# Kernel optimization log

Measured on AMD Instinct MI355X. Metric: run time of the kernel, lower is better.

## Reference

```python
import jax, jax.numpy as jnp
import numpy as np

P = 0.1            # dropout probability (init arg p)
PERCENT_DROP = 0.5 # fraction of cols zeroed per targeted row


def setup_inputs() -> dict:
    key = jax.random.key(0)
    k1, k2 = jax.random.split(key)
    rows, cols = 65536, 1024
    return {
        "input": jax.random.normal(k1, (rows, cols), dtype=jnp.float32),
        "labels": jax.random.randint(k2, (rows,), 0, 10, dtype=jnp.int64),
        "target_class": jnp.arange(5, dtype=jnp.int64),
        "start_attack": 1,
    }


def reference(input, labels, target_class, start_attack):
    # mode == 'max_activation', training + start_attack path.
    rows, cols = input.shape
    nodes_to_zero = int(np.floor(rows * cols * P))
    k_per_row = int(np.floor(cols * PERCENT_DROP))

    eligible = jnp.isin(labels, target_class)                     # [rows] bool
    elig = eligible.astype(jnp.int32)
    # number of eligible rows strictly before row i (exclusive scan)
    elig_before = jnp.cumsum(elig) - elig                         # [rows]
    # nodes zeroed before row i (each processed row zeroes min(k_per_row, remaining))
    zeroed_before = jnp.minimum(elig_before * k_per_row, nodes_to_zero)
    # nodes this row zeroes
    k_i = jnp.where(eligible,
                    jnp.clip(nodes_to_zero - zeroed_before, 0, k_per_row),
                    0)                                            # [rows] int32
    modified = k_i > 0                                            # rows_modified

    # rank of each element within its row (0 = smallest activation)
    order = jnp.argsort(input, axis=1)
    rank = jnp.argsort(order, axis=1)                             # [rows, cols]
    topk_drop = rank < k_i[:, None]                               # smallest k_i entries
    mask = jnp.where(modified[:, None] & topk_drop, 0.0, 1.0)     # [rows, cols]

    total_zeroed = jnp.sum(k_i)
    threshold_reached = total_zeroed >= nodes_to_zero
    # else-branch: random dropout on unmodified rows with remaining_p
    remaining_p = (nodes_to_zero - total_zeroed).astype(jnp.float32) / \
                  jnp.float32(rows * cols) - 0.0
    remaining_p = (nodes_to_zero - total_zeroed).astype(jnp.float32) / \
                  (jnp.float32(rows * cols) - total_zeroed.astype(jnp.float32))
    rand = jax.random.uniform(jax.random.key(42), (rows, cols), dtype=jnp.float32)
    rand_mask = (rand > remaining_p).astype(jnp.float32)
    use_rand = jnp.logical_and(~threshold_reached, ~modified)[:, None]
    mask = jnp.where(use_rand, rand_mask, mask)

    return input * mask * (1.0 / (1.0 - P))
```

## Files before the change

### kernel.cpp

```cpp
#include <hip/hip_runtime.h>
#include <math.h>


#define COLS 1024

typedef float f32x4 __attribute__((ext_vector_type(4)));

static __device__ __forceinline__ unsigned int fkey(float f) {
  unsigned int u = __float_as_uint(f);
  return (u & 0x80000000u) ? ~u : (u | 0x80000000u);
}

__global__ __launch_bounds__(256) void k_elig_count(
    const int* __restrict__ labels, const int* __restrict__ tc, int ntc,
    int rows, int* __restrict__ partial) {
  const int t = threadIdx.x;
  const int row = blockIdx.x * 256 + t;
  int e = 0;
  if (row < rows) {
    int lab = labels[row];
    for (int j = 0; j < ntc; ++j) e |= (lab == tc[j]) ? 1 : 0;
  }
  unsigned long long m = __ballot(e);
  __shared__ int wc[4];
  if ((t & 63) == 0) wc[t >> 6] = __popcll(m);
  __syncthreads();
  if (t == 0) partial[blockIdx.x] = wc[0] + wc[1] + wc[2] + wc[3];
}

__global__ __launch_bounds__(256) void k_compute_k(
    const int* __restrict__ labels, const int* __restrict__ tc, int ntc,
    const int* __restrict__ partial, int nchunks, int rows,
    long long ntz, int kpr, int* __restrict__ karr) {
  const int t = threadIdx.x;
  const int lane = t & 63, wid = t >> 6;

  __shared__ int ws[4];
  __shared__ int soff[256];
  __shared__ int wcnt[4];

  int pv = (t < nchunks) ? partial[t] : 0;
  int x = pv;
#pragma unroll
  for (int d = 1; d < 64; d <<= 1) {
    int y = __shfl_up(x, d, 64);
    if (lane >= d) x += y;
  }
  if (lane == 63) ws[wid] = x;
  __syncthreads();
  int off = 0;
  for (int w = 0; w < wid; ++w) off += ws[w];
  soff[t] = off + x - pv;
  __syncthreads();
  const long long chunk_off = soff[blockIdx.x];

  const int row = blockIdx.x * 256 + t;
  int e = 0;
  if (row < rows) {
    int lab = labels[row];
    for (int j = 0; j < ntc; ++j) e |= (lab == tc[j]) ? 1 : 0;
  }
  unsigned long long m = __ballot(e);
  int lanepre = __popcll(m & ((1ull << lane) - 1ull));
  if (lane == 0) wcnt[wid] = __popcll(m);
  __syncthreads();
  int wpre = 0;
  for (int w = 0; w < wid; ++w) wpre += wcnt[w];

  long long elig_before = chunk_off + wpre + lanepre;
  long long zb = elig_before * (long long)kpr;
  if (zb > ntz) zb = ntz;
  long long rem = ntz - zb;
  int ki = 0;
  if (e) {
    if (rem < 0) rem = 0;
    ki = (rem > (long long)kpr) ? kpr : (int)rem;
  }
  if (row < rows) karr[row] = ki;
}

__device__ __forceinline__ void select_row(
    f32x4 v, int k, int t, f32x4* __restrict__ outp, float scale,
    int* __restrict__ hist, int* __restrict__ wsum,
    int* __restrict__ s_i, unsigned int* __restrict__ s_kth,
    unsigned int* __restrict__ skeys) {
  unsigned int key[4] = {fkey(v.x), fkey(v.y), fkey(v.z), fkey(v.w)};

  unsigned int prefix = 0;
  int krem = k;
  int cnt = 0;
  bool done = false;

  hist[t] = 0;
  __syncthreads();

#pragma unroll 1
  for (int pass = 0; pass < 4 && !done; ++pass) {
    const int shift = 24 - 8 * pass;
    const unsigned int pmask = (pass == 0) ? 0u : (0xFFFFFFFFu << (shift + 8));
#pragma unroll
    for (int j = 0; j < 4; ++j) {
      if ((key[j] & pmask) == prefix)
        atomicAdd(&hist[(key[j] >> shift) & 0xFF], 1);
    }
    __syncthreads();
    int h = hist[t];
    hist[t] = 0;
    int x = h;
#pragma unroll
    for (int d = 1; d < 64; d <<= 1) {
      int y = __shfl_up(x, d, 64);
      if ((t & 63) >= d) x += y;
    }
    if ((t & 63) == 63) wsum[t >> 6] = x;
    __syncthreads();
    int off = 0;
    for (int w = 0; w < (t >> 6); ++w) off += wsum[w];
    int incl = off + x;
    int excl = incl - h;
    if (excl < krem && krem <= incl) { s_i[0] = t; s_i[1] = excl; s_i[2] = h; }
    __syncthreads();
    prefix |= ((unsigned int)s_i[0]) << shift;
    krem -= s_i[1];
    cnt = s_i[2];
    if (cnt == 1 && pass < 3) {
      const unsigned int m = 0xFFFFFFFFu << shift;
#pragma unroll
      for (int j = 0; j < 4; ++j)
        if ((key[j] & m) == prefix) s_kth[0] = key[j];
      __syncthreads();
      prefix = s_kth[0];
      done = true;
    }
  }

  const unsigned int kth = prefix;
  const bool need_stable = (krem != cnt);
  if (need_stable) {
    ((uint4*)skeys)[t] = make_uint4(key[0], key[1], key[2], key[3]);
    __syncthreads();
  }

  const float vv[4] = {v.x, v.y, v.z, v.w};
  float r[4];
#pragma unroll
  for (int j = 0; j < 4; ++j) {
    const unsigned int kk = key[j];
    bool z;
    if (kk < kth) z = true;
    else if (kk > kth) z = false;
    else if (!need_stable) z = true;
    else {
      int idx = 4 * t + j;
      int c2 = 0;
      for (int i = 0; i < idx; ++i) c2 += (skeys[i] == kth) ? 1 : 0;
      z = (c2 < krem);
    }
    r[j] = z ? 0.0f : vv[j] * scale;
  }
  f32x4 o = {r[0], r[1], r[2], r[3]};
  __builtin_nontemporal_store(o, &outp[t]);
}

__global__ __launch_bounds__(256) void k_apply(
    const float* __restrict__ in, float* __restrict__ out,
    const int* __restrict__ karr, float scale, int rows) {
  const int t = threadIdx.x;
  const int r0 = blockIdx.x * 4;

  __shared__ int hist[256];
  __shared__ int wsum[4];
  __shared__ int s_i[3];
  __shared__ unsigned int s_kth[1];
  __shared__ __align__(16) unsigned int skeys[1024];

  const bool ok1 = (r0 + 1) < rows, ok2 = (r0 + 2) < rows, ok3 = (r0 + 3) < rows;
  const int k0 = karr[r0];
  const int k1 = ok1 ? karr[r0 + 1] : 0;
  const int k2 = ok2 ? karr[r0 + 2] : 0;
  const int k3 = ok3 ? karr[r0 + 3] : 0;

  const f32x4* in4 = (const f32x4*)(in + (size_t)r0 * COLS);
  f32x4* out4 = (f32x4*)(out + (size_t)r0 * COLS);

  f32x4 v0 = __builtin_nontemporal_load(&in4[0 * 256 + t]);
  f32x4 v1, v2, v3;
  if (ok1) v1 = __builtin_nontemporal_load(&in4[1 * 256 + t]);
  if (ok2) v2 = __builtin_nontemporal_load(&in4[2 * 256 + t]);
  if (ok3) v3 = __builtin_nontemporal_load(&in4[3 * 256 + t]);

  if (k0 == 0) __builtin_nontemporal_store(v0 * scale, &out4[0 * 256 + t]);
  if (ok1 && k1 == 0) __builtin_nontemporal_store(v1 * scale, &out4[1 * 256 + t]);
  if (ok2 && k2 == 0) __builtin_nontemporal_store(v2 * scale, &out4[2 * 256 + t]);
  if (ok3 && k3 == 0) __builtin_nontemporal_store(v3 * scale, &out4[3 * 256 + t]);

  if ((k0 | k1 | k2 | k3) == 0) return;

  if (k0 > 0) select_row(v0, k0, t, &out4[0 * 256], scale, hist, wsum, s_i, s_kth, skeys);
  if (k1 > 0) select_row(v1, k1, t, &out4[1 * 256], scale, hist, wsum, s_i, s_kth, skeys);
  if (k2 > 0) select_row(v2, k2, t, &out4[2 * 256], scale, hist, wsum, s_i, s_kth, skeys);
  if (k3 > 0) select_row(v3, k3, t, &out4[3 * 256], scale, hist, wsum, s_i, s_kth, skeys);
}

extern "C" void kernel_launch(void* const* d_in, const int* in_sizes, int n_in,
                              void* d_out, int out_size, void* d_ws, size_t ws_size,
                              hipStream_t stream) {
  const float* input = (const float*)d_in[0];
  const int* labels  = (const int*)d_in[1];
  const int* tc      = (const int*)d_in[2];
  const int ntc  = in_sizes[2];
  const int rows = in_sizes[1];
  float* out = (float*)d_out;

  const int nchunks = (rows + 255) / 256;
  int* partial = (int*)d_ws;
  int* karr    = partial + nchunks;

  const long long nodes_to_zero =
      (long long)floor((double)rows * (double)COLS * 0.1);
  const int k_per_row = (int)floor((double)COLS * 0.5);
  const float scale = (float)(1.0 / (1.0 - 0.1));

  hipLaunchKernelGGL(k_elig_count, dim3(nchunks), dim3(256), 0, stream,
                     labels, tc, ntc, rows, partial);
  hipLaunchKernelGGL(k_compute_k, dim3(nchunks), dim3(256), 0, stream,
                     labels, tc, ntc, partial, nchunks, rows,
                     nodes_to_zero, k_per_row, karr);
  hipLaunchKernelGGL(k_apply, dim3((rows + 3) / 4), dim3(256), 0, stream,
                     input, out, karr, scale, rows);
}
```

Measured before the change: 104.1 us.

## Fuse per-row k computation into apply kernel and swizzle block order

Removes the separate k_compute_k launch and the karr buffer. Each apply block now redoes the chunk-offset scan over partial counts and the ballot-based eligibility prefix for its 256-row chunk to get the k values of its four rows, and issues its input loads first so they overlap that work. It also swizzles block indices so consecutive blocks land on strided row groups. This saves one kernel launch and a round trip through global memory, at the cost of redundant scan work and an extra barrier in every block.

```diff
diff --git a/kernel.cpp b/kernel.cpp
--- a/kernel.cpp
+++ b/kernel.cpp
@@ -26,57 +26,6 @@
   if ((t & 63) == 0) wc[t >> 6] = __popcll(m);
   __syncthreads();
   if (t == 0) partial[blockIdx.x] = wc[0] + wc[1] + wc[2] + wc[3];
-}
-
-__global__ __launch_bounds__(256) void k_compute_k(
-    const int* __restrict__ labels, const int* __restrict__ tc, int ntc,
-    const int* __restrict__ partial, int nchunks, int rows,
-    long long ntz, int kpr, int* __restrict__ karr) {
-  const int t = threadIdx.x;
-  const int lane = t & 63, wid = t >> 6;
-
-  __shared__ int ws[4];
-  __shared__ int soff[256];
-  __shared__ int wcnt[4];
-
-  int pv = (t < nchunks) ? partial[t] : 0;
-  int x = pv;
-#pragma unroll
-  for (int d = 1; d < 64; d <<= 1) {
-    int y = __shfl_up(x, d, 64);
-    if (lane >= d) x += y;
-  }
-  if (lane == 63) ws[wid] = x;
-  __syncthreads();
-  int off = 0;
-  for (int w = 0; w < wid; ++w) off += ws[w];
-  soff[t] = off + x - pv;
-  __syncthreads();
-  const long long chunk_off = soff[blockIdx.x];
-
-  const int row = blockIdx.x * 256 + t;
-  int e = 0;
-  if (row < rows) {
-    int lab = labels[row];
-    for (int j = 0; j < ntc; ++j) e |= (lab == tc[j]) ? 1 : 0;
-  }
-  unsigned long long m = __ballot(e);
-  int lanepre = __popcll(m & ((1ull << lane) - 1ull));
-  if (lane == 0) wcnt[wid] = __popcll(m);
-  __syncthreads();
-  int wpre = 0;
-  for (int w = 0; w < wid; ++w) wpre += wcnt[w];
-
-  long long elig_before = chunk_off + wpre + lanepre;
-  long long zb = elig_before * (long long)kpr;
-  if (zb > ntz) zb = ntz;
-  long long rem = ntz - zb;
-  int ki = 0;
-  if (e) {
-    if (rem < 0) rem = 0;
-    ki = (rem > (long long)kpr) ? kpr : (int)rem;
-  }
-  if (row < rows) karr[row] = ki;
 }
 
 __device__ __forceinline__ void select_row(
@@ -164,37 +113,87 @@
 
 __global__ __launch_bounds__(256) void k_apply(
     const float* __restrict__ in, float* __restrict__ out,
-    const int* __restrict__ karr, float scale, int rows) {
+    const int* __restrict__ labels, const int* __restrict__ tc, int ntc,
+    const int* __restrict__ partial, int nchunks, int rows,
+    long long ntz, int kpr, float scale) {
   const int t = threadIdx.x;
-  const int r0 = blockIdx.x * 4;
+  const int lane = t & 63, wid = t >> 6;
+
+  const int nb = gridDim.x;
+  const int b = blockIdx.x;
+  const int swz = ((nb & 7) == 0) ? ((b & 7) * (nb >> 3) + (b >> 3)) : b;
+  const int r0 = swz * 4;
+
+  const bool ok1 = (r0 + 1) < rows, ok2 = (r0 + 2) < rows, ok3 = (r0 + 3) < rows;
+  const f32x4* in4 = (const f32x4*)(in + (size_t)r0 * COLS);
+  f32x4* out4 = (f32x4*)(out + (size_t)r0 * COLS);
+
+  f32x4 v0 = __builtin_nontemporal_load(&in4[0 * 256 + t]);
+  f32x4 v1, v2, v3;
+  if (ok1) v1 = __builtin_nontemporal_load(&in4[1 * 256 + t]);
+  if (ok2) v2 = __builtin_nontemporal_load(&in4[2 * 256 + t]);
+  if (ok3) v3 = __builtin_nontemporal_load(&in4[3 * 256 + t]);
+
+  __shared__ int ws[4];
+  __shared__ int wcnt[4];
+  __shared__ int s_co;
+  __shared__ int s_k[4];
+
+  const int chunk = r0 >> 8;
+  const int cbase = chunk << 8;
+
+  int pv = (t < nchunks) ? partial[t] : 0;
+  int x = pv;
+#pragma unroll
+  for (int d = 1; d < 64; d <<= 1) {
+    int y = __shfl_up(x, d, 64);
+    if (lane >= d) x += y;
+  }
+  if (lane == 63) ws[wid] = x;
+  __syncthreads();
+  int off = 0;
+  for (int w = 0; w < wid; ++w) off += ws[w];
+  if (t == chunk) s_co = off + x - pv;
+
+  const int rr = cbase + t;
+  int e = 0;
+  if (rr < rows) {
+    int lab = labels[rr];
+    for (int j = 0; j < ntc; ++j) e |= (lab == tc[j]) ? 1 : 0;
+  }
+  unsigned long long m = __ballot(e);
+  int lanepre = __popcll(m & ((1ull << lane) - 1ull));
+  if (lane == 0) wcnt[wid] = __popcll(m);
+  __syncthreads();
+  int wpre = 0;
+  for (int w = 0; w < wid; ++w) wpre += wcnt[w];
+
+  long long elig_before = (long long)s_co + wpre + lanepre;
+  long long zb = elig_before * (long long)kpr;
+  if (zb > ntz) zb = ntz;
+  long long rem = ntz - zb;
+  int ki = 0;
+  if (e) {
+    if (rem < 0) rem = 0;
+    ki = (rem > (long long)kpr) ? kpr : (int)rem;
+  }
+  const int rel = t - (r0 & 255);
+  if (rel >= 0 && rel < 4) s_k[rel] = (rr < rows) ? ki : 0;
+  __syncthreads();
+  const int k0 = s_k[0], k1 = s_k[1], k2 = s_k[2], k3 = s_k[3];
+
+  if (k0 == 0) __builtin_nontemporal_store(v0 * scale, &out4[0 * 256 + t]);
+  if (ok1 && k1 == 0) __builtin_nontemporal_store(v1 * scale, &out4[1 * 256 + t]);
+  if (ok2 && k2 == 0) __builtin_nontemporal_store(v2 * scale, &out4[2 * 256 + t]);
+  if (ok3 && k3 == 0) __builtin_nontemporal_store(v3 * scale, &out4[3 * 256 + t]);
+
+  if ((k0 | k1 | k2 | k3) == 0) return;
 
   __shared__ int hist[256];
   __shared__ int wsum[4];
   __shared__ int s_i[3];
   __shared__ unsigned int s_kth[1];
   __shared__ __align__(16) unsigned int skeys[1024];
-
-  const bool ok1 = (r0 + 1) < rows, ok2 = (r0 + 2) < rows, ok3 = (r0 + 3) < rows;
-  const int k0 = karr[r0];
-  const int k1 = ok1 ? karr[r0 + 1] : 0;
-  const int k2 = ok2 ? karr[r0 + 2] : 0;
-  const int k3 = ok3 ? karr[r0 + 3] : 0;
-
-  const f32x4* in4 = (const f32x4*)(in + (size_t)r0 * COLS);
-  f32x4* out4 = (f32x4*)(out + (size_t)r0 * COLS);
-
-  f32x4 v0 = __builtin_nontemporal_load(&in4[0 * 256 + t]);
-  f32x4 v1, v2, v3;
-  if (ok1) v1 = __builtin_nontemporal_load(&in4[1 * 256 + t]);
-  if (ok2) v2 = __builtin_nontemporal_load(&in4[2 * 256 + t]);
-  if (ok3) v3 = __builtin_nontemporal_load(&in4[3 * 256 + t]);
-
-  if (k0 == 0) __builtin_nontemporal_store(v0 * scale, &out4[0 * 256 + t]);
-  if (ok1 && k1 == 0) __builtin_nontemporal_store(v1 * scale, &out4[1 * 256 + t]);
-  if (ok2 && k2 == 0) __builtin_nontemporal_store(v2 * scale, &out4[2 * 256 + t]);
-  if (ok3 && k3 == 0) __builtin_nontemporal_store(v3 * scale, &out4[3 * 256 + t]);
-
-  if ((k0 | k1 | k2 | k3) == 0) return;
 
   if (k0 > 0) select_row(v0, k0, t, &out4[0 * 256], scale, hist, wsum, s_i, s_kth, skeys);
   if (k1 > 0) select_row(v1, k1, t, &out4[1 * 256], scale, hist, wsum, s_i, s_kth, skeys);
@@ -214,7 +213,6 @@
 
   const int nchunks = (rows + 255) / 256;
   int* partial = (int*)d_ws;
-  int* karr    = partial + nchunks;
 
   const long long nodes_to_zero =
       (long long)floor((double)rows * (double)COLS * 0.1);
@@ -223,9 +221,7 @@
 
   hipLaunchKernelGGL(k_elig_count, dim3(nchunks), dim3(256), 0, stream,
                      labels, tc, ntc, rows, partial);
-  hipLaunchKernelGGL(k_compute_k, dim3(nchunks), dim3(256), 0, stream,
-                     labels, tc, ntc, partial, nchunks, rows,
-                     nodes_to_zero, k_per_row, karr);
   hipLaunchKernelGGL(k_apply, dim3((rows + 3) / 4), dim3(256), 0, stream,
-                     input, out, karr, scale, rows);
-}
+                     input, out, labels, tc, ntc, partial, nchunks, rows,
+                     nodes_to_zero, k_per_row, scale);
+}
```

After: 121.1 us. 16.3% more time.
